# Kernel optimization log

Hardware: AMD Instinct MI355X
Metric: run time of the kernel (lower is better)

## Reference

```python
import jax, jax.numpy as jnp
import numpy as np

N_NODES = 100000
N_EDGES = 1600000
IN_DIM = 64
EMBED_DIM = 128
OUT_DIM = 10


def setup_inputs() -> dict:
    key = jax.random.key(0)
    ks = jax.random.split(key, 12)
    x = jax.random.normal(ks[0], (N_NODES, IN_DIM), dtype=jnp.float32)
    edge_index = jax.random.randint(ks[1], (2, N_EDGES), 0, N_NODES, dtype=jnp.int64)
    s = lambda k, shp, fan_in: jax.random.normal(k, shp, dtype=jnp.float32) / np.sqrt(fan_in)
    # SAGEConv params: lin_l (applied to aggregated neighbors, has bias), lin_r (root, no bias)
    W_l = s(ks[2], (IN_DIM, EMBED_DIM), IN_DIM)
    b_l = jnp.zeros((EMBED_DIM,), dtype=jnp.float32)
    W_r = s(ks[3], (IN_DIM, EMBED_DIM), IN_DIM)
    # Classifier MLP: embed -> 64 -> 128 -> out
    W1 = s(ks[4], (EMBED_DIM, 64), EMBED_DIM)
    b1 = jnp.zeros((64,), dtype=jnp.float32)
    W2 = s(ks[5], (64, 128), 64)
    b2 = jnp.zeros((128,), dtype=jnp.float32)
    W3 = s(ks[6], (128, OUT_DIM), 128)
    b3 = jnp.zeros((OUT_DIM,), dtype=jnp.float32)
    return {"x": x, "edge_index": edge_index, "W_l": W_l, "b_l": b_l, "W_r": W_r,
            "W1": W1, "b1": b1, "W2": W2, "b2": b2, "W3": W3, "b3": b3}


def reference(x, edge_index, W_l, b_l, W_r, W1, b1, W2, b2, W3, b3):
    src, dst = edge_index[0], edge_index[1]
    # mean-aggregate neighbor features: gather x[src], scatter-sum to dst, divide by degree
    msg = x[src]                                                   # [E, in_dim]
    agg = jax.ops.segment_sum(msg, dst, num_segments=N_NODES)      # [N, in_dim]
    deg = jax.ops.segment_sum(jnp.ones((src.shape[0],), x.dtype), dst, num_segments=N_NODES)
    mean = agg / jnp.maximum(deg, 1.0)[:, None]                    # [N, in_dim]
    # SAGEConv: lin_l(mean_neigh) + lin_r(x_root)
    h = mean @ W_l + b_l + x @ W_r                                 # [N, embed_dim]
    # classifier MLP (logits)
    h = jax.nn.relu(h @ W1 + b1)
    h = jax.nn.relu(h @ W2 + b2)
    return h @ W3 + b3
```

## Files before the change

### kernel.cpp

```cpp
#include <hip/hip_runtime.h>
#include <hip/hip_bf16.h>

#define N_NODES 100000
#define IN_DIM 64
#define EMB 128
#define HID1 64
#define HID2 128
#define OUT_DIM 10

#define CHUNK 4096
#define EPT   (CHUNK / 256)
#define NBUCK ((N_NODES + 511) >> 9)
#define CAPB 9216

#define NB_CONV ((N_NODES * 16) / 256)
#define WCAT_N (128 * 128)
#define W1T_N  (64 * 128)
#define W2T_N  (128 * 64)
#define W3T_N  (16 * 128)
#define PREP_TOT (WCAT_N + W1T_N + W2T_N + W3T_N)
#define NB_PREP ((PREP_TOT + 255) / 256)

using short8 = __attribute__((ext_vector_type(8))) short;
using bfx4   = __attribute__((ext_vector_type(4))) short;
using f32x4  = __attribute__((ext_vector_type(4))) float;

__device__ inline short f2bf(float f) {
  __hip_bfloat16 h = __float2bfloat16(f);
  return *reinterpret_cast<short*>(&h);
}

struct BinShared {
  int hist[256], excl[256], cur[256], gb[256];
  int stage[CHUNK];
  unsigned char bof[CHUNK];
  int sc[256];
};

__global__ __launch_bounds__(256) void frontend_kernel(
    const float* __restrict__ x,
    const int* __restrict__ src, const int* __restrict__ dst,
    const float* __restrict__ W_l, const float* __restrict__ W_r,
    const float* __restrict__ W1, const float* __restrict__ W2,
    const float* __restrict__ W3,
    int* __restrict__ gcur, int* __restrict__ ebuf, short* __restrict__ xb,
    short* __restrict__ wcat_t, short* __restrict__ w1t,
    short* __restrict__ w2t, short* __restrict__ w3t,
    int E, int nbC)
{
  __shared__ __align__(16) char smem_raw[sizeof(BinShared)];
  const int b = blockIdx.x;
  const int tid = threadIdx.x;

  if (b < nbC) {
    BinShared& S = *reinterpret_cast<BinShared*>(smem_raw);
    const int base = b * CHUNK;
    const int cn = min(CHUNK, E - base);

    int dreg[EPT];
#pragma unroll
    for (int it = 0; it < EPT; ++it) {
      int i = tid + it * 256;
      dreg[it] = (i < cn) ? dst[base + i] : -1;
    }

    S.hist[tid] = 0;
    __syncthreads();
#pragma unroll
    for (int it = 0; it < EPT; ++it)
      if (dreg[it] >= 0) atomicAdd(&S.hist[dreg[it] >> 9], 1);
    __syncthreads();

    int v = (tid < NBUCK) ? S.hist[tid] : 0;
    S.sc[tid] = v;
    __syncthreads();
    for (int off = 1; off < 256; off <<= 1) {
      int u = (tid >= off) ? S.sc[tid - off] : 0;
      __syncthreads();
      S.sc[tid] += u;
      __syncthreads();
    }
    {
      int ex = S.sc[tid] - v;
      S.excl[tid] = ex; S.cur[tid] = ex;
      S.gb[tid] = (tid < NBUCK && v) ? atomicAdd(&gcur[tid], v) : 0;
    }
    __syncthreads();

#pragma unroll
    for (int it = 0; it < EPT; ++it) {
      int i = tid + it * 256;
      if (i < cn) {
        int d = dreg[it], s = src[base + i];
        int bk = d >> 9;
        int pos = atomicAdd(&S.cur[bk], 1);
        S.stage[pos] = ((d & 511) << 17) | s;
        S.bof[pos] = (unsigned char)bk;
      }
    }
    __syncthreads();

    for (int i = tid; i < cn; i += 256) {
      int bk = S.bof[i];
      int idx = S.gb[bk] + (i - S.excl[bk]);
      if (idx < CAPB) ebuf[bk * CAPB + idx] = S.stage[i];
    }
  } else if (b < nbC + NB_CONV) {
    int t = (b - nbC) * 256 + tid;
    int node = t >> 4, g = t & 15;
    f32x4 v = *(const f32x4*)&x[(size_t)node * IN_DIM + g * 4];
    bfx4 s;
#pragma unroll
    for (int i = 0; i < 4; ++i) s[i] = f2bf(v[i]);
    *(bfx4*)&xb[((size_t)node << 6) + g * 4] = s;
  } else {
    int t = (b - nbC - NB_CONV) * 256 + tid;
    if (t < WCAT_N) {
      int c = t >> 7, k = t & 127;
      float v = (k < 64) ? W_r[k * EMB + c] : W_l[(k - 64) * EMB + c];
      wcat_t[c * 128 + k] = f2bf(v);
    } else if (t < WCAT_N + W1T_N) {
      int u = t - WCAT_N;
      int c = u >> 7, k = u & 127;
      w1t[c * 128 + k] = f2bf(W1[k * HID1 + c]);
    } else if (t < WCAT_N + W1T_N + W2T_N) {
      int u = t - WCAT_N - W1T_N;
      int c = u >> 6, k = u & 63;
      w2t[c * 64 + k] = f2bf(W2[k * HID2 + c]);
    } else if (t < PREP_TOT) {
      int u = t - WCAT_N - W1T_N - W2T_N;
      int c = u >> 7, k = u & 127;
      w3t[c * 128 + k] = (c < OUT_DIM) ? f2bf(W3[k * OUT_DIM + c]) : (short)0;
    }
  }
}

__global__ __launch_bounds__(256) void bucket_csr(
    const int* __restrict__ gcur, int* __restrict__ ebuf,
    int* __restrict__ offs, int* __restrict__ oend)
{
  __shared__ int cnt[512], cur[512], sc[512];
  __shared__ int ep[CAPB];
  __shared__ int es[CAPB];
  const int b = blockIdx.x, tid = threadIdx.x;
  const int node0 = b << 9;
  const int nn = min(512, N_NODES - node0);
  const int ebase = b * CAPB;
  const int ecnt = min(gcur[b], CAPB);

  for (int i = tid; i < 512; i += 256) cnt[i] = 0;
  __syncthreads();
  for (int i = tid; i < ecnt; i += 256) {
    int p = ebuf[ebase + i];
    ep[i] = p;
    atomicAdd(&cnt[p >> 17], 1);
  }
  __syncthreads();
  for (int i = tid; i < 512; i += 256) sc[i] = cnt[i];
  __syncthreads();
  for (int off = 1; off < 512; off <<= 1) {
    int i0 = tid, i1 = tid + 256;
    int v0 = (i0 >= off) ? sc[i0 - off] : 0;
    int v1 = (i1 >= off) ? sc[i1 - off] : 0;
    __syncthreads();
    sc[i0] += v0; sc[i1] += v1;
    __syncthreads();
  }
  for (int i = tid; i < 512; i += 256) {
    int ex = sc[i] - cnt[i];
    cur[i] = ex;
    if (i < nn) {
      offs[node0 + i] = ebase + ex;
      oend[node0 + i] = ebase + sc[i];
    }
  }
  __syncthreads();
  for (int i = tid; i < ecnt; i += 256) {
    int p = ep[i];
    int pos = atomicAdd(&cur[p >> 17], 1);
    es[pos] = p & 131071;
  }
  __syncthreads();
  for (int i = tid; i < ecnt; i += 256) ebuf[ebase + i] = es[i];
}

__global__ __launch_bounds__(256) void aggregate_kernel(
    const int* __restrict__ offs, const int* __restrict__ oend,
    const int* __restrict__ esrc, const short* __restrict__ xb,
    short* __restrict__ mb)
{
  int wv = (int)((blockIdx.x * 256 + threadIdx.x) >> 6);
  const int lane = threadIdx.x & 63;
  const int node = __builtin_amdgcn_readfirstlane(wv);
  if (node >= N_NODES) return;
  const int beg = offs[node];
  const int end = oend[node];
  const int deg = end - beg;
  const unsigned short* cb = (const unsigned short*)xb;
  float a = 0.f;

  int k = beg;
  for (; k + 16 <= end; k += 16) {
    unsigned o0  = ((unsigned)esrc[k]      << 6) + lane;
    unsigned o1  = ((unsigned)esrc[k + 1]  << 6) + lane;
    unsigned o2  = ((unsigned)esrc[k + 2]  << 6) + lane;
    unsigned o3  = ((unsigned)esrc[k + 3]  << 6) + lane;
    unsigned o4  = ((unsigned)esrc[k + 4]  << 6) + lane;
    unsigned o5  = ((unsigned)esrc[k + 5]  << 6) + lane;
    unsigned o6  = ((unsigned)esrc[k + 6]  << 6) + lane;
    unsigned o7  = ((unsigned)esrc[k + 7]  << 6) + lane;
    unsigned o8  = ((unsigned)esrc[k + 8]  << 6) + lane;
    unsigned o9  = ((unsigned)esrc[k + 9]  << 6) + lane;
    unsigned o10 = ((unsigned)esrc[k + 10] << 6) + lane;
    unsigned o11 = ((unsigned)esrc[k + 11] << 6) + lane;
    unsigned o12 = ((unsigned)esrc[k + 12] << 6) + lane;
    unsigned o13 = ((unsigned)esrc[k + 13] << 6) + lane;
    unsigned o14 = ((unsigned)esrc[k + 14] << 6) + lane;
    unsigned o15 = ((unsigned)esrc[k + 15] << 6) + lane;
    unsigned u0  = cb[o0],  u1  = cb[o1],  u2  = cb[o2],  u3  = cb[o3];
    unsigned u4  = cb[o4],  u5  = cb[o5],  u6  = cb[o6],  u7  = cb[o7];
    unsigned u8  = cb[o8],  u9  = cb[o9],  u10 = cb[o10], u11 = cb[o11];
    unsigned u12 = cb[o12], u13 = cb[o13], u14 = cb[o14], u15 = cb[o15];
    a += __uint_as_float(u0  << 16); a += __uint_as_float(u1  << 16);
    a += __uint_as_float(u2  << 16); a += __uint_as_float(u3  << 16);
    a += __uint_as_float(u4  << 16); a += __uint_as_float(u5  << 16);
    a += __uint_as_float(u6  << 16); a += __uint_as_float(u7  << 16);
    a += __uint_as_float(u8  << 16); a += __uint_as_float(u9  << 16);
    a += __uint_as_float(u10 << 16); a += __uint_as_float(u11 << 16);
    a += __uint_as_float(u12 << 16); a += __uint_as_float(u13 << 16);
    a += __uint_as_float(u14 << 16); a += __uint_as_float(u15 << 16);
  }
  if (k + 8 <= end) {
    unsigned o0 = ((unsigned)esrc[k]     << 6) + lane;
    unsigned o1 = ((unsigned)esrc[k + 1] << 6) + lane;
    unsigned o2 = ((unsigned)esrc[k + 2] << 6) + lane;
    unsigned o3 = ((unsigned)esrc[k + 3] << 6) + lane;
    unsigned o4 = ((unsigned)esrc[k + 4] << 6) + lane;
    unsigned o5 = ((unsigned)esrc[k + 5] << 6) + lane;
    unsigned o6 = ((unsigned)esrc[k + 6] << 6) + lane;
    unsigned o7 = ((unsigned)esrc[k + 7] << 6) + lane;
    unsigned u0 = cb[o0], u1 = cb[o1], u2 = cb[o2], u3 = cb[o3];
    unsigned u4 = cb[o4], u5 = cb[o5], u6 = cb[o6], u7 = cb[o7];
    a += __uint_as_float(u0 << 16); a += __uint_as_float(u1 << 16);
    a += __uint_as_float(u2 << 16); a += __uint_as_float(u3 << 16);
    a += __uint_as_float(u4 << 16); a += __uint_as_float(u5 << 16);
    a += __uint_as_float(u6 << 16); a += __uint_as_float(u7 << 16);
    k += 8;
  }
  if (k + 4 <= end) {
    unsigned o0 = ((unsigned)esrc[k]     << 6) + lane;
    unsigned o1 = ((unsigned)esrc[k + 1] << 6) + lane;
    unsigned o2 = ((unsigned)esrc[k + 2] << 6) + lane;
    unsigned o3 = ((unsigned)esrc[k + 3] << 6) + lane;
    unsigned u0 = cb[o0], u1 = cb[o1], u2 = cb[o2], u3 = cb[o3];
    a += __uint_as_float(u0 << 16); a += __uint_as_float(u1 << 16);
    a += __uint_as_float(u2 << 16); a += __uint_as_float(u3 << 16);
    k += 4;
  }
  for (; k < end; ++k) {
    unsigned u0 = cb[((unsigned)esrc[k] << 6) + lane];
    a += __uint_as_float(u0 << 16);
  }

  float m = a / fmaxf((float)deg, 1.0f);
  ((unsigned short*)mb)[((size_t)node << 6) + lane] = (unsigned short)f2bf(m);
}

#define PA 128
#define PH 64

__global__ __launch_bounds__(256) void fused_mfma_kernel(
    const short* __restrict__ xb, const short* __restrict__ mb,
    const short* __restrict__ wcat_t, const short* __restrict__ w1t,
    const short* __restrict__ w2t, const short* __restrict__ w3t,
    const float* __restrict__ b_l, const float* __restrict__ b1,
    const float* __restrict__ b2, const float* __restrict__ b3,
    float* __restrict__ out)
{
  __shared__ __align__(16) short sA0[64 * PA];
  __shared__ __align__(16) short sH [64 * PA];
  __shared__ __align__(16) short sH1[64 * PH];
  __shared__ __align__(16) short sW [128 * PA];

  const int tid  = threadIdx.x;
  const int base = blockIdx.x * 64;
  const int lane = tid & 63;
  const int w    = tid >> 6;
  const int lrow = lane & 15;
  const int lgrp = lane >> 4;

  for (int T = tid; T < 1024; T += 256) {
    int n = T >> 4, g = T & 15;
    int node = base + n;
    short8 s = {0, 0, 0, 0, 0, 0, 0, 0};
    if (node < N_NODES) {
      const short* sp = (g < 8) ? &xb[((size_t)node << 6) + 8 * g]
                                : &mb[((size_t)node << 6) + 8 * (g - 8)];
      s = *(const short8*)sp;
    }
    *(short8*)&sA0[(n * PA + 8 * g) ^ ((n & 7) << 3)] = s;
  }
  for (int T = tid; T < 2048; T += 256) {
    int c = T >> 4, kg = T & 15;
    *(short8*)&sW[(c * PA + 8 * kg) ^ ((c & 7) << 3)] =
        *(const short8*)&wcat_t[c * 128 + 8 * kg];
  }
  __syncthreads();

  {
    const int c0w = 32 * w;
    short8 bf[2][4];
#pragma unroll
    for (int ct = 0; ct < 2; ++ct)
#pragma unroll
      for (int kk = 0; kk < 4; ++kk) {
        int row = c0w + 16 * ct + lrow;
        bf[ct][kk] = *(const short8*)&sW[(row * PA + kk * 32 + lgrp * 8) ^ ((row & 7) << 3)];
      }
#pragma unroll
    for (int rt = 0; rt < 4; ++rt) {
      short8 af[4];
#pragma unroll
      for (int kk = 0; kk < 4; ++kk) {
        int row = rt * 16 + lrow;
        af[kk] = *(const short8*)&sA0[(row * PA + kk * 32 + lgrp * 8) ^ ((row & 7) << 3)];
      }
#pragma unroll
      for (int ct = 0; ct < 2; ++ct) {
        float bv = b_l[c0w + 16 * ct + lrow];
        f32x4 acc = {bv, bv, bv, bv};
#pragma unroll
        for (int kk = 0; kk < 4; ++kk)
          acc = __builtin_amdgcn_mfma_f32_16x16x32_bf16(af[kk], bf[ct][kk], acc, 0, 0, 0);
        int col = c0w + 16 * ct + lrow;
        int rb = rt * 16 + lgrp * 4;
#pragma unroll
        for (int r = 0; r < 4; ++r) {
          int row = rb + r;
          sH[(row * PA + col) ^ ((row & 7) << 3)] = f2bf(acc[r]);
        }
      }
    }
  }
  __syncthreads();

  for (int T = tid; T < 1024; T += 256) {
    int c = T >> 4, kg = T & 15;
    *(short8*)&sW[(c * PA + 8 * kg) ^ ((c & 7) << 3)] =
        *(const short8*)&w1t[c * 128 + 8 * kg];
  }
  {
    int c = tid >> 4, kg = tid & 15;
    *(short8*)&sA0[(c * PA + 8 * kg) ^ ((c & 7) << 3)] =
        *(const short8*)&w3t[c * 128 + 8 * kg];
  }
  __syncthreads();

  {
    const int c0 = 16 * w;
    short8 bf[4];
#pragma unroll
    for (int kk = 0; kk < 4; ++kk) {
      int row = c0 + lrow;
      bf[kk] = *(const short8*)&sW[(row * PA + kk * 32 + lgrp * 8) ^ ((row & 7) << 3)];
    }
#pragma unroll
    for (int rt = 0; rt < 4; ++rt) {
      short8 af[4];
#pragma unroll
      for (int kk = 0; kk < 4; ++kk) {
        int row = rt * 16 + lrow;
        af[kk] = *(const short8*)&sH[(row * PA + kk * 32 + lgrp * 8) ^ ((row & 7) << 3)];
      }
      float bv = b1[c0 + lrow];
      f32x4 acc = {bv, bv, bv, bv};
#pragma unroll
      for (int kk = 0; kk < 4; ++kk)
        acc = __builtin_amdgcn_mfma_f32_16x16x32_bf16(af[kk], bf[kk], acc, 0, 0, 0);
      int col = c0 + lrow;
      int rb = rt * 16 + lgrp * 4;
#pragma unroll
      for (int r = 0; r < 4; ++r) {
        int row = rb + r;
        sH1[(row * PH + col) ^ ((row & 7) << 3)] = f2bf(fmaxf(acc[r], 0.f));
      }
    }
  }
  __syncthreads();

  for (int T = tid; T < 1024; T += 256) {
    int c = T >> 3, kg = T & 7;
    *(short8*)&sW[(c * PA + 8 * kg) ^ ((c & 7) << 3)] =
        *(const short8*)&w2t[c * 64 + 8 * kg];
  }
  __syncthreads();

  {
    const int c0w = 32 * w;
    short8 bf[2][2];
#pragma unroll
    for (int ct = 0; ct < 2; ++ct)
#pragma unroll
      for (int kk = 0; kk < 2; ++kk) {
        int row = c0w + 16 * ct + lrow;
        bf[ct][kk] = *(const short8*)&sW[(row * PA + kk * 32 + lgrp * 8) ^ ((row & 7) << 3)];
      }
#pragma unroll
    for (int rt = 0; rt < 4; ++rt) {
      short8 af[2];
#pragma unroll
      for (int kk = 0; kk < 2; ++kk) {
        int row = rt * 16 + lrow;
        af[kk] = *(const short8*)&sH1[(row * PH + kk * 32 + lgrp * 8) ^ ((row & 7) << 3)];
      }
#pragma unroll
      for (int ct = 0; ct < 2; ++ct) {
        float bv = b2[c0w + 16 * ct + lrow];
        f32x4 acc = {bv, bv, bv, bv};
#pragma unroll
        for (int kk = 0; kk < 2; ++kk)
          acc = __builtin_amdgcn_mfma_f32_16x16x32_bf16(af[kk], bf[ct][kk], acc, 0, 0, 0);
        int col = c0w + 16 * ct + lrow;
        int rb = rt * 16 + lgrp * 4;
#pragma unroll
        for (int r = 0; r < 4; ++r) {
          int row = rb + r;
          sH[(row * PA + col) ^ ((row & 7) << 3)] = f2bf(fmaxf(acc[r], 0.f));
        }
      }
    }
  }
  __syncthreads();

  {
    short8 af[4], bf[4];
#pragma unroll
    for (int kk = 0; kk < 4; ++kk) {
      int row = 16 * w + lrow;
      af[kk] = *(const short8*)&sH[(row * PA + kk * 32 + lgrp * 8) ^ ((row & 7) << 3)];
      bf[kk] = *(const short8*)&sA0[(lrow * PA + kk * 32 + lgrp * 8) ^ ((lrow & 7) << 3)];
    }
    float bv = (lrow < OUT_DIM) ? b3[lrow] : 0.f;
    f32x4 acc = {bv, bv, bv, bv};
#pragma unroll
    for (int kk = 0; kk < 4; ++kk)
      acc = __builtin_amdgcn_mfma_f32_16x16x32_bf16(af[kk], bf[kk], acc, 0, 0, 0);
#pragma unroll
    for (int r = 0; r < 4; ++r) {
      int row = 16 * w + lgrp * 4 + r;
      int node = base + row;
      if (node < N_NODES && lrow < OUT_DIM)
        out[(long long)node * OUT_DIM + lrow] = acc[r];
    }
  }
}

extern "C" void kernel_launch(void* const* d_in, const int* in_sizes, int n_in,
                              void* d_out, int out_size, void* d_ws, size_t ws_size,
                              hipStream_t stream) {
  const float* x   = (const float*)d_in[0];
  const int*   ei  = (const int*)d_in[1];
  const float* W_l = (const float*)d_in[2];
  const float* b_l = (const float*)d_in[3];
  const float* W_r = (const float*)d_in[4];
  const float* W1  = (const float*)d_in[5];
  const float* b1  = (const float*)d_in[6];
  const float* W2  = (const float*)d_in[7];
  const float* b2  = (const float*)d_in[8];
  const float* W3  = (const float*)d_in[9];
  const float* b3  = (const float*)d_in[10];
  float* out = (float*)d_out;

  const int E = in_sizes[1] / 2;
  const int* src = ei;
  const int* dst = ei + E;

  short* wcat_t = (short*)d_ws;
  short* w1t    = wcat_t + WCAT_N;
  short* w2t    = w1t + W1T_N;
  short* w3t    = w2t + W2T_N;
  short* xb     = w3t + W3T_N;
  short* mb     = xb + (size_t)N_NODES * 64;
  int*   offs   = (int*)(mb + (size_t)N_NODES * 64);
  int*   oend   = offs + N_NODES;
  int*   ebuf   = oend + N_NODES;
  int*   gcur   = ebuf + (size_t)NBUCK * CAPB;

  (void)hipMemsetAsync(gcur, 0, NBUCK * sizeof(int), stream);

  const int nbC = (E + CHUNK - 1) / CHUNK;
  frontend_kernel<<<nbC + NB_CONV + NB_PREP, 256, 0, stream>>>(
      x, src, dst, W_l, W_r, W1, W2, W3,
      gcur, ebuf, xb, wcat_t, w1t, w2t, w3t, E, nbC);

  bucket_csr<<<NBUCK, 256, 0, stream>>>(gcur, ebuf, offs, oend);

  int nbAgg = (N_NODES * 64 + 255) / 256;
  aggregate_kernel<<<nbAgg, 256, 0, stream>>>(offs, oend, ebuf, xb, mb);

  int nbF = (N_NODES + 63) / 64;
  fused_mfma_kernel<<<nbF, 256, 0, stream>>>(xb, mb, wcat_t, w1t, w2t, w3t,
                                             b_l, b1, b2, b3, out);
}
```

Measured before the change: 110.7 us.

## Load MLP weight fragments directly from global memory and halve aggregation chunk

The fused MLP kernel no longer stages weight matrices into shared memory. Each wave now reads its B fragments straight from global (L2-cached) weights, which removes the 32 KB sW buffer, the weight-copy loops and two block barriers, and should allow more blocks per CU. Separately, the aggregation chunk size drops from 4096 to 2048 edges, giving more, smaller blocks in the scatter stage. The trade-off is more global/L2 traffic per block for weights, and more blocks with their own per-block overhead in aggregation.

```diff
diff --git a/kernel.cpp b/kernel.cpp
--- a/kernel.cpp
+++ b/kernel.cpp
@@ -8,7 +8,7 @@
 #define HID2 128
 #define OUT_DIM 10
 
-#define CHUNK 4096
+#define CHUNK 2048
 #define EPT   (CHUNK / 256)
 #define NBUCK ((N_NODES + 511) >> 9)
 #define CAPB 9216
@@ -280,7 +280,6 @@
   __shared__ __align__(16) short sA0[64 * PA];
   __shared__ __align__(16) short sH [64 * PA];
   __shared__ __align__(16) short sH1[64 * PH];
-  __shared__ __align__(16) short sW [128 * PA];
 
   const int tid  = threadIdx.x;
   const int base = blockIdx.x * 64;
@@ -300,11 +299,6 @@
     }
     *(short8*)&sA0[(n * PA + 8 * g) ^ ((n & 7) << 3)] = s;
   }
-  for (int T = tid; T < 2048; T += 256) {
-    int c = T >> 4, kg = T & 15;
-    *(short8*)&sW[(c * PA + 8 * kg) ^ ((c & 7) << 3)] =
-        *(const short8*)&wcat_t[c * 128 + 8 * kg];
-  }
   __syncthreads();
 
   {
@@ -315,7 +309,7 @@
 #pragma unroll
       for (int kk = 0; kk < 4; ++kk) {
         int row = c0w + 16 * ct + lrow;
-        bf[ct][kk] = *(const short8*)&sW[(row * PA + kk * 32 + lgrp * 8) ^ ((row & 7) << 3)];
+        bf[ct][kk] = *(const short8*)&wcat_t[row * 128 + kk * 32 + lgrp * 8];
       }
 #pragma unroll
     for (int rt = 0; rt < 4; ++rt) {
@@ -344,25 +338,13 @@
   }
   __syncthreads();
 
-  for (int T = tid; T < 1024; T += 256) {
-    int c = T >> 4, kg = T & 15;
-    *(short8*)&sW[(c * PA + 8 * kg) ^ ((c & 7) << 3)] =
-        *(const short8*)&w1t[c * 128 + 8 * kg];
-  }
-  {
-    int c = tid >> 4, kg = tid & 15;
-    *(short8*)&sA0[(c * PA + 8 * kg) ^ ((c & 7) << 3)] =
-        *(const short8*)&w3t[c * 128 + 8 * kg];
-  }
-  __syncthreads();
-
   {
     const int c0 = 16 * w;
     short8 bf[4];
 #pragma unroll
     for (int kk = 0; kk < 4; ++kk) {
       int row = c0 + lrow;
-      bf[kk] = *(const short8*)&sW[(row * PA + kk * 32 + lgrp * 8) ^ ((row & 7) << 3)];
+      bf[kk] = *(const short8*)&w1t[row * 128 + kk * 32 + lgrp * 8];
     }
 #pragma unroll
     for (int rt = 0; rt < 4; ++rt) {
@@ -388,13 +370,6 @@
   }
   __syncthreads();
 
-  for (int T = tid; T < 1024; T += 256) {
-    int c = T >> 3, kg = T & 7;
-    *(short8*)&sW[(c * PA + 8 * kg) ^ ((c & 7) << 3)] =
-        *(const short8*)&w2t[c * 64 + 8 * kg];
-  }
-  __syncthreads();
-
   {
     const int c0w = 32 * w;
     short8 bf[2][2];
@@ -403,7 +378,7 @@
 #pragma unroll
       for (int kk = 0; kk < 2; ++kk) {
         int row = c0w + 16 * ct + lrow;
-        bf[ct][kk] = *(const short8*)&sW[(row * PA + kk * 32 + lgrp * 8) ^ ((row & 7) << 3)];
+        bf[ct][kk] = *(const short8*)&w2t[row * 64 + kk * 32 + lgrp * 8];
       }
 #pragma unroll
     for (int rt = 0; rt < 4; ++rt) {
@@ -438,7 +413,7 @@
     for (int kk = 0; kk < 4; ++kk) {
       int row = 16 * w + lrow;
       af[kk] = *(const short8*)&sH[(row * PA + kk * 32 + lgrp * 8) ^ ((row & 7) << 3)];
-      bf[kk] = *(const short8*)&sA0[(lrow * PA + kk * 32 + lgrp * 8) ^ ((lrow & 7) << 3)];
+      bf[kk] = *(const short8*)&w3t[lrow * 128 + kk * 32 + lgrp * 8];
     }
     float bv = (lrow < OUT_DIM) ? b3[lrow] : 0.f;
     f32x4 acc = {bv, bv, bv, bv};
```

Result: no change. 111.1 us (+0.4%).
